# Optimization experiments

Measured on AMD Instinct MI355X. Metric: run time of the kernel, lower is better.

## Reference

```python
import jax, jax.numpy as jnp
import numpy as np

B = 4194304  # batch
H = 32       # hidden width of TinyMLP


def _xavier(key, fan_in, fan_out, gain=0.5):
    lim = gain * np.sqrt(6.0 / (fan_in + fan_out))
    return jax.random.uniform(key, (fan_in, fan_out), jnp.float32, -lim, lim)


def setup_inputs() -> dict:
    key = jax.random.key(0)
    ks = jax.random.split(key, 7)
    return {
        "x1": jax.random.normal(ks[0], (B,), jnp.float32),
        "x2": jax.random.normal(ks[1], (B,), jnp.float32),
        "y1": jax.random.normal(ks[2], (B,), jnp.float32),
        "y2": jax.random.normal(ks[3], (B,), jnp.float32),
        "W1": _xavier(ks[4], 2, H),
        "b1": jnp.zeros((H,), jnp.float32),
        "W2": _xavier(ks[5], H, H),
        "b2": jnp.zeros((H,), jnp.float32),
        "W3": _xavier(ks[6], H, 1),
        "b3": jnp.zeros((1,), jnp.float32),
    }


def reference(x1, x2, y1, y2, W1, b1, W2, b2, W3, b3):
    # Y: [B, 2]
    Y = jnp.stack([y1, y2], axis=1)

    def F_sum(Yv):
        h1 = jax.nn.sigmoid(Yv @ W1 + b1)   # [B, H]
        h2 = jax.nn.sigmoid(h1 @ W2 + b2)   # [B, H]
        return jnp.sum(h2 @ W3 + b3)        # scalar sum of F values

    dF_dY = jax.grad(F_sum)(Y)              # [B, 2], analytic input-gradient

    x1_out = x1 + dF_dY[:, 0]
    x2_out = x2 + dF_dY[:, 1]
    # Stack the 4 output streams as columns: (x1', x2', y1, y2)
    return jnp.stack([x1_out, x2_out, y1, y2], axis=1)
```

## Files before the change

kernel.cpp:

```cpp
#include <hip/hip_runtime.h>


#define H 32
#define NLOG2E (-1.4426950408889634f)

typedef __attribute__((ext_vector_type(8))) short bf16x8;
typedef __attribute__((ext_vector_type(16))) float f32x16;
typedef __attribute__((ext_vector_type(4))) float f32x4;
typedef __attribute__((ext_vector_type(2))) float f32x2;
typedef __attribute__((ext_vector_type(2))) __bf16 bfx2;

#define MFMA32 __builtin_amdgcn_mfma_f32_32x32x16_bf16

__device__ __forceinline__ int cvt_pk_bf16(float a, float b) {
    f32x2 f; f[0] = a; f[1] = b;
    bfx2 r = __builtin_convertvector(f, bfx2);
    return __builtin_bit_cast(int, r);
}
__device__ __forceinline__ float pklo(int p) {
    unsigned u = (unsigned)p << 16; return __builtin_bit_cast(float, u);
}
__device__ __forceinline__ float pkhi(int p) {
    unsigned u = (unsigned)p & 0xFFFF0000u; return __builtin_bit_cast(float, u);
}

__device__ __forceinline__ f32x4 rcp4(const f32x4 a) {
    float m01 = a[0] * a[1], m23 = a[2] * a[3];
    float r   = __builtin_amdgcn_rcpf(m01 * m23);
    float r01 = r * m23, r23 = r * m01;
    f32x4 s; s[0] = a[1] * r01; s[1] = a[0] * r01; s[2] = a[3] * r23; s[3] = a[2] * r23;
    return s;
}

__global__ __launch_bounds__(256, 6) void tinymlp_mfma_kernel(
    const float* __restrict__ x1, const float* __restrict__ x2,
    const float* __restrict__ y1, const float* __restrict__ y2,
    const float* __restrict__ W1, const float* __restrict__ b1,
    const float* __restrict__ W2, const float* __restrict__ b2,
    const float* __restrict__ W3,
    float4* __restrict__ out, int ntiles)
{
    __shared__ unsigned short lds0[8192];

    const int tid  = threadIdx.x;
    const int w    = tid >> 6;
    const int lane = tid & 63;
    const int n    = lane & 31;
    const int q5   = lane >> 5;

    union U4 { int i[4]; bf16x8 v; };
    U4 A_z1, A_z2a, A_z2b, A_dh1a, A_dh1b, A_dya, A_dyb;

    #pragma unroll
    for (int t = 0; t < 4; ++t) {
        const int j0 = 8 * q5 + 2 * t;
        const int j1 = j0 + 1;
        A_z2a.i[t] = cvt_pk_bf16(NLOG2E * W2[j0 * H + n],        NLOG2E * W2[j1 * H + n]);
        A_z2b.i[t] = cvt_pk_bf16(NLOG2E * W2[(16 + j0) * H + n], NLOG2E * W2[(16 + j1) * H + n]);
        A_dh1a.i[t] = cvt_pk_bf16(W2[n * H + j0] * W3[j0],           W2[n * H + j1] * W3[j1]);
        A_dh1b.i[t] = cvt_pk_bf16(W2[n * H + 16 + j0] * W3[16 + j0], W2[n * H + 16 + j1] * W3[16 + j1]);
        A_dya.i[t] = (n < 2) ? cvt_pk_bf16(W1[n * H + j0],      W1[n * H + j1])      : 0;
        A_dyb.i[t] = (n < 2) ? cvt_pk_bf16(W1[n * H + 16 + j0], W1[n * H + 16 + j1]) : 0;
    }

    A_z1.i[0] = A_z1.i[1] = A_z1.i[2] = A_z1.i[3] = 0;
    if (q5 == 0) {
        const float wa = NLOG2E * W1[n];
        const float wb = NLOG2E * W1[H + n];
        const float bv = NLOG2E * b1[n];
        const int hi  = cvt_pk_bf16(wa, wb);
        const int lo  = cvt_pk_bf16(wa - pklo(hi), wb - pkhi(hi));
        const int bh  = cvt_pk_bf16(bv, 0.f);
        const int bhl = cvt_pk_bf16(bv, bv - pklo(bh));
        A_z1.i[0] = hi; A_z1.i[1] = lo; A_z1.i[2] = hi; A_z1.i[3] = bhl;
    }

    f32x16 b2C;
    #pragma unroll
    for (int t = 0; t < 4; ++t) {
        const float4 bt = *(const float4*)&b2[8 * t + 4 * q5];
        b2C[4 * t + 0] = NLOG2E * bt.x; b2C[4 * t + 1] = NLOG2E * bt.y;
        b2C[4 * t + 2] = NLOG2E * bt.z; b2C[4 * t + 3] = NLOG2E * bt.w;
    }

    f32x16 zf16;
    #pragma unroll
    for (int r = 0; r < 16; ++r) zf16[r] = 0.f;

    unsigned short*       wb = &lds0[w * 2048 + n * 8 + q5 * 4];
    const unsigned short* rb = &lds0[w * 2048 + q5 * 256 + n * 8];

    const int gwave  = (blockIdx.x * blockDim.x + tid) >> 6;
    const int nwaves = (gridDim.x * blockDim.x) >> 6;
    unsigned idx = (unsigned)gwave * 32 + (unsigned)n;
    const unsigned step = (unsigned)nwaves * 32;

    for (int tt = gwave; tt < ntiles; tt += nwaves) {
        float y1v = 0.f, y2v = 0.f;
        if (lane < 32) { y1v = y1[idx]; y2v = y2[idx]; }

        U4 uY;
        const int pkHI = cvt_pk_bf16(y1v, y2v);
        const int pkLO = cvt_pk_bf16(y1v - pklo(pkHI), y2v - pkhi(pkHI));
        uY.i[0] = pkHI; uY.i[1] = pkHI; uY.i[2] = pkLO;
        uY.i[3] = (lane < 32) ? 0x3F803F80 : 0;

        const f32x16 acc = MFMA32(A_z1.v, uY.v, zf16, 0, 0, 0);

        int P[8];
        #pragma unroll
        for (int t = 0; t < 4; ++t) {
            f32x4 e;
            #pragma unroll
            for (int r = 0; r < 4; ++r) e[r] = __builtin_amdgcn_exp2f(acc[4 * t + r]);
            e += 1.0f;
            const f32x4 s = rcp4(e);
            P[2 * t]     = cvt_pk_bf16(s[0], s[1]);
            P[2 * t + 1] = cvt_pk_bf16(s[2], s[3]);
            int2 v; v.x = P[2 * t]; v.y = P[2 * t + 1];
            *(int2*)(wb + t * 256) = v;
        }
        __builtin_amdgcn_wave_barrier();

        const bf16x8 B1 = *(const bf16x8*)rb;
        const bf16x8 B2 = *(const bf16x8*)(rb + 512);
        f32x16 zz = MFMA32(A_z2a.v, B1, b2C, 0, 0, 0);
        zz = MFMA32(A_z2b.v, B2, zz, 0, 0, 0);

        #pragma unroll
        for (int t = 0; t < 4; ++t) {
            f32x4 e;
            #pragma unroll
            for (int r = 0; r < 4; ++r) e[r] = __builtin_amdgcn_exp2f(zz[4 * t + r]);
            e += 1.0f;
            const f32x4 s = rcp4(e);
            f32x2 sv;
            sv[0] = s[0]; sv[1] = s[1];
            sv = __builtin_elementwise_fma(-sv, sv, sv);
            const int q0 = cvt_pk_bf16(sv[0], sv[1]);
            sv[0] = s[2]; sv[1] = s[3];
            sv = __builtin_elementwise_fma(-sv, sv, sv);
            const int q1 = cvt_pk_bf16(sv[0], sv[1]);
            int2 v; v.x = q0; v.y = q1;
            *(int2*)(wb + 1024 + t * 256) = v;
        }
        __builtin_amdgcn_wave_barrier();

        float xv1 = 0.f, xv2 = 0.f;
        if (lane < 32) { xv1 = x1[idx]; xv2 = x2[idx]; }

        const bf16x8 D1 = *(const bf16x8*)(rb + 1024);
        const bf16x8 D2 = *(const bf16x8*)(rb + 1536);
        f32x16 dh = MFMA32(A_dh1a.v, D1, zf16, 0, 0, 0);
        dh = MFMA32(A_dh1b.v, D2, dh, 0, 0, 0);

        #pragma unroll
        for (int t = 0; t < 4; ++t) {
            f32x2 sv, gg;
            sv[0] = pklo(P[2 * t]); sv[1] = pkhi(P[2 * t]);
            sv = __builtin_elementwise_fma(-sv, sv, sv);
            gg[0] = dh[4 * t]; gg[1] = dh[4 * t + 1]; gg *= sv;
            const int g0 = cvt_pk_bf16(gg[0], gg[1]);
            sv[0] = pklo(P[2 * t + 1]); sv[1] = pkhi(P[2 * t + 1]);
            sv = __builtin_elementwise_fma(-sv, sv, sv);
            gg[0] = dh[4 * t + 2]; gg[1] = dh[4 * t + 3]; gg *= sv;
            const int g1 = cvt_pk_bf16(gg[0], gg[1]);
            int2 v; v.x = g0; v.y = g1;
            *(int2*)(wb + t * 256) = v;
        }
        __builtin_amdgcn_wave_barrier();

        const bf16x8 E1 = *(const bf16x8*)rb;
        const bf16x8 E2 = *(const bf16x8*)(rb + 512);
        f32x16 ay = MFMA32(A_dya.v, E1, zf16, 0, 0, 0);
        ay = MFMA32(A_dyb.v, E2, ay, 0, 0, 0);

        if (lane < 32) {
            float4 o;
            o.x = xv1 + ay[0];
            o.y = xv2 + ay[1];
            o.z = y1v;
            o.w = y2v;
            out[idx] = o;
        }
        __builtin_amdgcn_wave_barrier();

        idx += step;
    }
}

extern "C" void kernel_launch(void* const* d_in, const int* in_sizes, int n_in,
                              void* d_out, int out_size, void* d_ws, size_t ws_size,
                              hipStream_t stream) {
    const float* x1 = (const float*)d_in[0];
    const float* x2 = (const float*)d_in[1];
    const float* y1 = (const float*)d_in[2];
    const float* y2 = (const float*)d_in[3];
    const float* W1 = (const float*)d_in[4];
    const float* b1 = (const float*)d_in[5];
    const float* W2 = (const float*)d_in[6];
    const float* b2 = (const float*)d_in[7];
    const float* W3 = (const float*)d_in[8];

    const int n = in_sizes[0];
    const int ntiles = n / 32;
    const int block = 256;
    const int grid = 1536;
    tinymlp_mfma_kernel<<<grid, block, 0, stream>>>(
        x1, x2, y1, y2, W1, b1, W2, b2, W3, (float4*)d_out, ntiles);
}
```

Before: 203.9 us.

## Replace LDS transposes between MFMA stages with v_permlane32_swap register shuffles

The kernel no longer stages MFMA outputs through shared memory to reshape them into B operands for the next MFMA. Each tile now uses v_permlane32_swap to exchange register halves between the two 32-lane groups, which removes LDS writes, reads and the wave barriers between stages. The x1/x2 loads are also hoisted to the top of the loop so they overlap with compute. This relies on the swap producing exactly the operand layout that the LDS round-trip produced. Upper-half lanes now feed the bias-ones column as well, but their results are never stored.

New measurement: 205.5 us. No clear change (+0.7%).

```diff
diff --git a/kernel.cpp b/kernel.cpp
--- a/kernel.cpp
+++ b/kernel.cpp
@@ -22,6 +22,10 @@
 }
 __device__ __forceinline__ float pkhi(int p) {
     unsigned u = (unsigned)p & 0xFFFF0000u; return __builtin_bit_cast(float, u);
+}
+
+__device__ __forceinline__ void plane32_swap(int &d, int &s) {
+    asm volatile("v_permlane32_swap_b32 %0, %1" : "+v"(d), "+v"(s));
 }
 
 __device__ __forceinline__ f32x4 rcp4(const f32x4 a) {
@@ -40,10 +44,7 @@
     const float* __restrict__ W3,
     float4* __restrict__ out, int ntiles)
 {
-    __shared__ unsigned short lds0[8192];
-
     const int tid  = threadIdx.x;
-    const int w    = tid >> 6;
     const int lane = tid & 63;
     const int n    = lane & 31;
     const int q5   = lane >> 5;
@@ -87,23 +88,23 @@
     #pragma unroll
     for (int r = 0; r < 16; ++r) zf16[r] = 0.f;
 
-    unsigned short*       wb = &lds0[w * 2048 + n * 8 + q5 * 4];
-    const unsigned short* rb = &lds0[w * 2048 + q5 * 256 + n * 8];
-
     const int gwave  = (blockIdx.x * blockDim.x + tid) >> 6;
     const int nwaves = (gridDim.x * blockDim.x) >> 6;
     unsigned idx = (unsigned)gwave * 32 + (unsigned)n;
     const unsigned step = (unsigned)nwaves * 32;
 
     for (int tt = gwave; tt < ntiles; tt += nwaves) {
-        float y1v = 0.f, y2v = 0.f;
-        if (lane < 32) { y1v = y1[idx]; y2v = y2[idx]; }
+        float y1v = 0.f, y2v = 0.f, xv1 = 0.f, xv2 = 0.f;
+        if (lane < 32) {
+            y1v = y1[idx]; y2v = y2[idx];
+            xv1 = x1[idx]; xv2 = x2[idx];
+        }
 
         U4 uY;
         const int pkHI = cvt_pk_bf16(y1v, y2v);
         const int pkLO = cvt_pk_bf16(y1v - pklo(pkHI), y2v - pkhi(pkHI));
         uY.i[0] = pkHI; uY.i[1] = pkHI; uY.i[2] = pkLO;
-        uY.i[3] = (lane < 32) ? 0x3F803F80 : 0;
+        uY.i[3] = 0x3F803F80;
 
         const f32x16 acc = MFMA32(A_z1.v, uY.v, zf16, 0, 0, 0);
 
@@ -117,16 +118,22 @@
             const f32x4 s = rcp4(e);
             P[2 * t]     = cvt_pk_bf16(s[0], s[1]);
             P[2 * t + 1] = cvt_pk_bf16(s[2], s[3]);
-            int2 v; v.x = P[2 * t]; v.y = P[2 * t + 1];
-            *(int2*)(wb + t * 256) = v;
-        }
-        __builtin_amdgcn_wave_barrier();
-
-        const bf16x8 B1 = *(const bf16x8*)rb;
-        const bf16x8 B2 = *(const bf16x8*)(rb + 512);
-        f32x16 zz = MFMA32(A_z2a.v, B1, b2C, 0, 0, 0);
-        zz = MFMA32(A_z2b.v, B2, zz, 0, 0, 0);
-
+        }
+
+        U4 B1f, B2f;
+        {
+            int a0 = P[0], a2 = P[2]; plane32_swap(a0, a2);
+            int a1 = P[1], a3 = P[3]; plane32_swap(a1, a3);
+            B1f.i[0] = a0; B1f.i[1] = a1; B1f.i[2] = a2; B1f.i[3] = a3;
+            int b0 = P[4], b2i = P[6]; plane32_swap(b0, b2i);
+            int b1i = P[5], b3 = P[7]; plane32_swap(b1i, b3);
+            B2f.i[0] = b0; B2f.i[1] = b1i; B2f.i[2] = b2i; B2f.i[3] = b3;
+        }
+
+        f32x16 zz = MFMA32(A_z2a.v, B1f.v, b2C, 0, 0, 0);
+        zz = MFMA32(A_z2b.v, B2f.v, zz, 0, 0, 0);
+
+        int Q[8];
         #pragma unroll
         for (int t = 0; t < 4; ++t) {
             f32x4 e;
@@ -137,43 +144,47 @@
             f32x2 sv;
             sv[0] = s[0]; sv[1] = s[1];
             sv = __builtin_elementwise_fma(-sv, sv, sv);
-            const int q0 = cvt_pk_bf16(sv[0], sv[1]);
+            Q[2 * t] = cvt_pk_bf16(sv[0], sv[1]);
             sv[0] = s[2]; sv[1] = s[3];
             sv = __builtin_elementwise_fma(-sv, sv, sv);
-            const int q1 = cvt_pk_bf16(sv[0], sv[1]);
-            int2 v; v.x = q0; v.y = q1;
-            *(int2*)(wb + 1024 + t * 256) = v;
-        }
-        __builtin_amdgcn_wave_barrier();
-
-        float xv1 = 0.f, xv2 = 0.f;
-        if (lane < 32) { xv1 = x1[idx]; xv2 = x2[idx]; }
-
-        const bf16x8 D1 = *(const bf16x8*)(rb + 1024);
-        const bf16x8 D2 = *(const bf16x8*)(rb + 1536);
-        f32x16 dh = MFMA32(A_dh1a.v, D1, zf16, 0, 0, 0);
-        dh = MFMA32(A_dh1b.v, D2, dh, 0, 0, 0);
-
+            Q[2 * t + 1] = cvt_pk_bf16(sv[0], sv[1]);
+        }
+
+        U4 D1f, D2f;
+        plane32_swap(Q[0], Q[2]);
+        plane32_swap(Q[1], Q[3]);
+        D1f.i[0] = Q[0]; D1f.i[1] = Q[1]; D1f.i[2] = Q[2]; D1f.i[3] = Q[3];
+        plane32_swap(Q[4], Q[6]);
+        plane32_swap(Q[5], Q[7]);
+        D2f.i[0] = Q[4]; D2f.i[1] = Q[5]; D2f.i[2] = Q[6]; D2f.i[3] = Q[7];
+
+        f32x16 dh = MFMA32(A_dh1a.v, D1f.v, zf16, 0, 0, 0);
+        dh = MFMA32(A_dh1b.v, D2f.v, dh, 0, 0, 0);
+
+        int G[8];
         #pragma unroll
         for (int t = 0; t < 4; ++t) {
             f32x2 sv, gg;
             sv[0] = pklo(P[2 * t]); sv[1] = pkhi(P[2 * t]);
             sv = __builtin_elementwise_fma(-sv, sv, sv);
             gg[0] = dh[4 * t]; gg[1] = dh[4 * t + 1]; gg *= sv;
-            const int g0 = cvt_pk_bf16(gg[0], gg[1]);
+            G[2 * t] = cvt_pk_bf16(gg[0], gg[1]);
             sv[0] = pklo(P[2 * t + 1]); sv[1] = pkhi(P[2 * t + 1]);
             sv = __builtin_elementwise_fma(-sv, sv, sv);
             gg[0] = dh[4 * t + 2]; gg[1] = dh[4 * t + 3]; gg *= sv;
-            const int g1 = cvt_pk_bf16(gg[0], gg[1]);
-            int2 v; v.x = g0; v.y = g1;
-            *(int2*)(wb + t * 256) = v;
-        }
-        __builtin_amdgcn_wave_barrier();
-
-        const bf16x8 E1 = *(const bf16x8*)rb;
-        const bf16x8 E2 = *(const bf16x8*)(rb + 512);
-        f32x16 ay = MFMA32(A_dya.v, E1, zf16, 0, 0, 0);
-        ay = MFMA32(A_dyb.v, E2, ay, 0, 0, 0);
+            G[2 * t + 1] = cvt_pk_bf16(gg[0], gg[1]);
+        }
+
+        U4 E1f, E2f;
+        plane32_swap(G[0], G[2]);
+        plane32_swap(G[1], G[3]);
+        E1f.i[0] = G[0]; E1f.i[1] = G[1]; E1f.i[2] = G[2]; E1f.i[3] = G[3];
+        plane32_swap(G[4], G[6]);
+        plane32_swap(G[5], G[7]);
+        E2f.i[0] = G[4]; E2f.i[1] = G[5]; E2f.i[2] = G[6]; E2f.i[3] = G[7];
+
+        f32x16 ay = MFMA32(A_dya.v, E1f.v, zf16, 0, 0, 0);
+        ay = MFMA32(A_dyb.v, E2f.v, ay, 0, 0, 0);
 
         if (lane < 32) {
             float4 o;
@@ -183,7 +194,6 @@
             o.w = y2v;
             out[idx] = o;
         }
-        __builtin_amdgcn_wave_barrier();
 
         idx += step;
     }
```
